# Performance work log

Measured on AMD Instinct MI355X. Metric: run time of the kernel, lower is better.

The kernel has to match this reference:

```python
import jax, jax.numpy as jnp
import numpy as np

B, S, HID = 2, 2048, 2048
NH, NKV, HD = 8, 1, 256
G = NH // NKV  # key-value groups
ROPE_BASE = 10000.0


def _rope_tables(seq_len, dim, base=ROPE_BASE):
    inv_freq = 1.0 / (base ** (jnp.arange(0, dim, 2, dtype=jnp.float32) / dim))
    t = jnp.arange(seq_len, dtype=jnp.float32)
    freqs = jnp.outer(t, inv_freq)            # [S, dim/2]
    emb = jnp.concatenate([freqs, freqs], -1)  # [S, dim]
    return jnp.cos(emb), jnp.sin(emb)


def _rotate_half(x):
    x1, x2 = jnp.split(x, 2, axis=-1)
    return jnp.concatenate([-x2, x1], axis=-1)


def setup_inputs() -> dict:
    key = jax.random.key(0)
    ks = jax.random.split(key, 6)
    hidden_states = jax.random.normal(ks[0], (B, S, HID), dtype=jnp.float32)
    # additive causal mask (0 on/below diagonal, -1e9 above)
    causal = jnp.triu(jnp.full((S, S), -1e9, dtype=jnp.float32), k=1)
    attention_mask = jnp.broadcast_to(causal[None, None], (B, 1, S, S))
    sc = 0.02
    Wq = jax.random.normal(ks[1], (HID, NH * HD), dtype=jnp.float32) * sc
    Wk = jax.random.normal(ks[2], (HID, NKV * HD), dtype=jnp.float32) * sc
    Wv = jax.random.normal(ks[3], (HID, NKV * HD), dtype=jnp.float32) * sc
    Wo = jax.random.normal(ks[4], (NH * HD, HID), dtype=jnp.float32) * sc
    return {"hidden_states": hidden_states, "attention_mask": attention_mask,
            "Wq": Wq, "Wk": Wk, "Wv": Wv, "Wo": Wo}


def reference(hidden_states, attention_mask, Wq, Wk, Wv, Wo):
    b, s, _ = hidden_states.shape
    q = (hidden_states @ Wq).reshape(b, s, NH, HD).transpose(0, 2, 1, 3)    # [B,NH,S,D]
    k = (hidden_states @ Wk).reshape(b, s, NKV, HD).transpose(0, 2, 1, 3)   # [B,NKV,S,D]
    v = (hidden_states @ Wv).reshape(b, s, NKV, HD).transpose(0, 2, 1, 3)
    cos, sin = _rope_tables(s, HD)
    cos, sin = cos[None, None], sin[None, None]
    q = q * cos + _rotate_half(q) * sin
    k = k * cos + _rotate_half(k) * sin
    # GQA: broadcast KV over groups instead of repeat_interleave (same math)
    qg = q.reshape(b, NKV, G, s, HD)
    scores = jnp.einsum('bkgqd,bkld->bkgql', qg, k) / np.sqrt(HD)  # [B,NKV,G,S,S]
    scores = scores + attention_mask[:, :, None]                    # mask broadcast over kv/groups
    probs = jax.nn.softmax(scores, axis=-1)
    out = jnp.einsum('bkgql,bkld->bkgqd', probs, v)                 # [B,NKV,G,S,D]
    out = out.reshape(b, NH, s, HD).transpose(0, 2, 1, 3).reshape(b, s, NH * HD)
    return out @ Wo
```

## Files before the change

kernel.cpp:

```cpp
#include <hip/hip_runtime.h>
#include <hip/hip_bf16.h>
#include <cstdint>
#include <cstddef>

#define DEVI __device__ __forceinline__

typedef __attribute__((ext_vector_type(8))) short short8;
typedef __attribute__((ext_vector_type(4))) float f32x4;

constexpr int BB = 2, SS = 2048, HID = 2048, NH = 8, HD = 256;
constexpr int M_TOT = BB * SS;
constexpr int RTOT = BB * NH * SS;
constexpr float SM_SCALE_LOG2 = 0.09016844005556021f;

DEVI unsigned short f2bf(float f) {
  union { float f; unsigned int u; } v; v.f = f;
  unsigned int u = v.u;
  unsigned int r = (u + 0x7FFFu + ((u >> 16) & 1u)) >> 16;
  return (unsigned short)r;
}

DEVI float bf2f(unsigned short u) {
  union { unsigned int i; float f; } v; v.i = ((unsigned int)u) << 16;
  return v.f;
}

DEVI void gload_lds16(const void* g, void* l) {
  __builtin_amdgcn_global_load_lds(
      (const __attribute__((address_space(1))) unsigned int*)g,
      (__attribute__((address_space(3))) unsigned int*)l, 16, 0, 0);
}

__global__ void convert_f32_bf16(const float* __restrict__ in,
                                 unsigned short* __restrict__ out, int n8) {
  const int i = blockIdx.x * blockDim.x + threadIdx.x;
  if (i >= n8) return;
  const f32x4* p = (const f32x4*)in;
  f32x4 a = p[i * 2], b = p[i * 2 + 1];
  short8 o;
#pragma unroll
  for (int j = 0; j < 4; ++j) {
    o[j] = (short)f2bf(a[j]);
    o[j + 4] = (short)f2bf(b[j]);
  }
  ((short8*)out)[i] = o;
}

__global__ void transpose_w(const float* __restrict__ W,
                            unsigned short* __restrict__ Wt, int K, int N) {
  __shared__ float t[32][33];
  const int n0 = blockIdx.x * 32, k0 = blockIdx.y * 32;
  const int c = threadIdx.x & 31, r8 = threadIdx.x >> 5;
#pragma unroll
  for (int i = 0; i < 4; ++i) {
    const int r = r8 + i * 8;
    t[r][c] = W[(size_t)(k0 + r) * N + n0 + c];
  }
  __syncthreads();
#pragma unroll
  for (int i = 0; i < 4; ++i) {
    const int r = r8 + i * 8;
    Wt[(size_t)(n0 + r) * K + k0 + c] = f2bf(t[c][r]);
  }
}

__global__ void rope_table(float* __restrict__ ct, float* __restrict__ st) {
  const int i = blockIdx.x * blockDim.x + threadIdx.x;
  const int s = i >> 7, d = i & 127;
  const float inv = __expf(-(float)d * (9.210340371976184f / 128.0f));
  const float ang = (float)s * inv;
  float sn, cs;
  sincosf(ang, &sn, &cs);
  ct[i] = cs;
  st[i] = sn;
}

__global__ void rope_apply8(unsigned short* __restrict__ X, const float* __restrict__ ct,
                            const float* __restrict__ st, int heads, int stride, int total16) {
  const int i = blockIdx.x * blockDim.x + threadIdx.x;
  if (i >= total16) return;
  const int d0 = (i & 15) * 8;
  const int t = i >> 4;
  const int hh = t % heads;
  const int row = t / heads;
  const int s = row & (SS - 1);
  const size_t base = (size_t)row * stride + (size_t)hh * HD + d0;
  short8 q1 = *(const short8*)&X[base];
  short8 q2 = *(const short8*)&X[base + 128];
  const float* ctr = ct + s * 128 + d0;
  const float* str = st + s * 128 + d0;
  f32x4 c0 = *(const f32x4*)ctr, c1 = *(const f32x4*)(ctr + 4);
  f32x4 s0 = *(const f32x4*)str, s1 = *(const f32x4*)(str + 4);
  short8 o1, o2;
#pragma unroll
  for (int j = 0; j < 8; ++j) {
    const float a = bf2f((unsigned short)q1[j]);
    const float b = bf2f((unsigned short)q2[j]);
    const float cs = (j < 4) ? c0[j] : c1[j - 4];
    const float sn = (j < 4) ? s0[j] : s1[j - 4];
    o1[j] = (short)f2bf(a * cs - b * sn);
    o2[j] = (short)f2bf(b * cs + a * sn);
  }
  *(short8*)&X[base] = o1;
  *(short8*)&X[base + 128] = o2;
}

template <int WMODE>
__global__ __launch_bounds__(256)
void gemm_bt(const unsigned short* __restrict__ A,
             const unsigned short* __restrict__ Bt,
             void* __restrict__ Cp, void* __restrict__ Cp2, void* __restrict__ Cp3,
             int N, int K) {
  __shared__ unsigned short As[128 * 64];
  __shared__ unsigned short Bs[128 * 64];
  const int tid = threadIdx.x;
  const int wid = tid >> 6, lane = tid & 63;
  const int wr = wid >> 1, wc = wid & 1;
  const int l15 = lane & 15, lg = lane >> 4;
  const unsigned lid = blockIdx.y * gridDim.x + blockIdx.x;
  const unsigned cpx = (gridDim.x * gridDim.y) >> 3;
  const unsigned swz = (lid & 7) * cpx + (lid >> 3);
  const int m0 = (int)(swz / gridDim.x) * 128, n0 = (int)(swz % gridDim.x) * 128;
  const int lrow = lane >> 3, lch = lane & 7;
  f32x4 acc[4][4];
#pragma unroll
  for (int i = 0; i < 4; ++i)
#pragma unroll
    for (int j = 0; j < 4; ++j) acc[i][j] = f32x4{0.f, 0.f, 0.f, 0.f};
  const unsigned short* Ab = A + (size_t)m0 * K;
  const unsigned short* Bb = Bt + (size_t)n0 * K;
  for (int k0 = 0; k0 < K; k0 += 64) {
    __syncthreads();
#pragma unroll
    for (int i = 0; i < 4; ++i) {
      const int r0 = wid * 32 + i * 8;
      const int r = r0 + lrow;
      gload_lds16(Ab + (size_t)r * K + k0 + ((lch ^ (r & 7)) * 8), &As[r0 * 64]);
      gload_lds16(Bb + (size_t)r * K + k0 + ((lch ^ (r & 7)) * 8), &Bs[r0 * 64]);
    }
    asm volatile("s_waitcnt vmcnt(0)" ::: "memory");
    __syncthreads();
#pragma unroll
    for (int kk = 0; kk < 2; ++kk) {
      short8 a[4], b[4];
#pragma unroll
      for (int m = 0; m < 4; ++m) {
        const int row = wr * 64 + m * 16 + l15;
        a[m] = *(const short8*)&As[row * 64 + (((kk * 4 + lg) ^ (row & 7)) * 8)];
      }
#pragma unroll
      for (int n = 0; n < 4; ++n) {
        const int row = wc * 64 + n * 16 + l15;
        b[n] = *(const short8*)&Bs[row * 64 + (((kk * 4 + lg) ^ (row & 7)) * 8)];
      }
#pragma unroll
      for (int m = 0; m < 4; ++m)
#pragma unroll
        for (int n = 0; n < 4; ++n)
          acc[m][n] = __builtin_amdgcn_mfma_f32_16x16x32_bf16(a[m], b[n], acc[m][n], 0, 0, 0);
    }
  }
  const int row0 = m0 + wr * 64 + lg * 4;
  const int col0 = n0 + wc * 64 + l15;
#pragma unroll
  for (int m = 0; m < 4; ++m)
#pragma unroll
    for (int n = 0; n < 4; ++n)
#pragma unroll
      for (int r = 0; r < 4; ++r) {
        const int row = row0 + m * 16 + r;
        const int col = col0 + n * 16;
        const float v = acc[m][n][r];
        if (WMODE == 1) {
          ((float*)Cp)[(size_t)row * N + col] = v;
        } else {
          if (col < 2048)
            ((unsigned short*)Cp)[(size_t)row * 2048 + col] = f2bf(v);
          else if (col < 2304)
            ((unsigned short*)Cp2)[(size_t)row * 256 + (col - 2048)] = f2bf(v);
          else
            ((unsigned short*)Cp3)[((size_t)((row >> 11) * HD + (col - 2304))) * SS + (row & (SS - 1))] = f2bf(v);
        }
      }
}

__global__ __launch_bounds__(512)
void attn_split(const unsigned short* __restrict__ Q,
                const unsigned short* __restrict__ Kc,
                const unsigned short* __restrict__ Vt,
                unsigned short* __restrict__ Opart, float* __restrict__ Ml) {
  __shared__ unsigned short Ks[2][64 * 256];
  __shared__ unsigned short Vs[2][256 * 64];
  __shared__ unsigned short Ps[8][1024];
  const int tid = threadIdx.x;
  const int wid = tid >> 6, lane = tid & 63;
  const int l15 = lane & 15, lg = lane >> 4;
  const int pi = (int)blockIdx.x >> 1, s = (int)blockIdx.x & 1;
  const int h = blockIdx.y, b = blockIdx.z;
  const int qtA = pi, qtB = 15 - pi;

  short8 qf[8];
  f32x4 acc[16];
  float mrow[4], lrow[4];

  auto load_q = [&](int qt) {
    const int qrow = qt * 128 + wid * 16 + l15;
    const size_t qbase = ((size_t)(b * SS + qrow)) * (NH * HD) + (size_t)h * HD;
#pragma unroll
    for (int c = 0; c < 8; ++c)
      qf[c] = *(const short8*)&Q[qbase + c * 32 + lg * 8];
#pragma unroll
    for (int n = 0; n < 16; ++n) acc[n] = f32x4{0.f, 0.f, 0.f, 0.f};
#pragma unroll
    for (int r = 0; r < 4; ++r) { mrow[r] = -3e38f; lrow[r] = 0.f; }
  };

  auto write_part = [&](int qt) {
    const size_t rbase = ((size_t)(b * NH + h)) * SS + qt * 128 + wid * 16 + lg * 4;
#pragma unroll
    for (int n = 0; n < 16; ++n)
#pragma unroll
      for (int r = 0; r < 4; ++r)
        Opart[((size_t)s * RTOT + rbase + r) * 256 + n * 16 + l15] = f2bf(acc[n][r]);
    if (l15 == 0) {
#pragma unroll
      for (int r = 0; r < 4; ++r)
        ((float2*)Ml)[(size_t)s * RTOT + rbase + r] = float2{mrow[r], lrow[r]};
    }
  };

  auto stage = [&](int buf, int kv0) {
    unsigned short* KsB = &Ks[buf][0];
    unsigned short* VsB = &Vs[buf][0];
#pragma unroll
    for (int j = 0; j < 4; ++j) {
      {
        const int r0 = wid * 8 + j * 2;
        const int r = r0 + (lane >> 5), c = lane & 31;
        gload_lds16(Kc + ((size_t)(b * SS + kv0 + r)) * HD + ((c ^ (r & 7)) * 8),
                    &KsB[r0 * 256]);
      }
      {
        const int r0 = (wid * 4 + j) * 8;
        const int r = r0 + (lane >> 3), c = lane & 7;
        gload_lds16(Vt + ((size_t)(b * HD + r)) * SS + kv0 + ((c ^ (r & 7)) * 8),
                    &VsB[r0 * 64]);
      }
    }
  };

  auto compute = [&](int buf, int qt, int kv0) {
    const int wmax = qt * 128 + wid * 16 + 15;
    if (kv0 > wmax) return;
    const unsigned short* KsB = &Ks[buf][0];
    const unsigned short* VsB = &Vs[buf][0];
    f32x4 sf[4];
    __builtin_amdgcn_s_setprio(1);
#pragma unroll
    for (int t = 0; t < 4; ++t) {
      f32x4 sv = {0.f, 0.f, 0.f, 0.f};
      const int kvr = t * 16 + l15;
      const char* krow = (const char*)KsB + kvr * 512;
      const int sw = (kvr & 7) << 4;
#pragma unroll
      for (int c = 0; c < 8; ++c) {
        short8 bf = *(const short8*)(krow + ((c * 64 + lg * 16) ^ sw));
        sv = __builtin_amdgcn_mfma_f32_16x16x32_bf16(qf[c], bf, sv, 0, 0, 0);
      }
      sf[t] = sv;
    }
    __builtin_amdgcn_s_setprio(0);

    float pm[4] = {-3e38f, -3e38f, -3e38f, -3e38f};
    const int qr0 = qt * 128 + wid * 16 + lg * 4;
#pragma unroll
    for (int t = 0; t < 4; ++t) {
      const int kvc = kv0 + t * 16 + l15;
#pragma unroll
      for (int r = 0; r < 4; ++r) {
        float v = sf[t][r] * SM_SCALE_LOG2;
        v = (kvc > qr0 + r) ? -3e38f : v;
        sf[t][r] = v;
        pm[r] = fmaxf(pm[r], v);
      }
    }
    float scale[4];
    float growth = -3e38f;
#pragma unroll
    for (int r = 0; r < 4; ++r) {
      float v = pm[r];
      v = fmaxf(v, __shfl_xor(v, 1));
      v = fmaxf(v, __shfl_xor(v, 2));
      v = fmaxf(v, __shfl_xor(v, 4));
      v = fmaxf(v, __shfl_xor(v, 8));
      pm[r] = v;
      growth = fmaxf(growth, v - mrow[r]);
    }
    const bool norescale = __all(growth <= 0.f);
#pragma unroll
    for (int r = 0; r < 4; ++r) {
      const float mn = norescale ? mrow[r] : fmaxf(mrow[r], pm[r]);
      scale[r] = norescale ? 1.f : exp2f(mrow[r] - mn);
      mrow[r] = mn;
      float sum = 0.f;
#pragma unroll
      for (int t = 0; t < 4; ++t) {
        const float p = exp2f(sf[t][r] - mn);
        sf[t][r] = p;
        sum += p;
      }
      sum += __shfl_xor(sum, 1);
      sum += __shfl_xor(sum, 2);
      sum += __shfl_xor(sum, 4);
      sum += __shfl_xor(sum, 8);
      lrow[r] = lrow[r] * scale[r] + sum;
    }
    if (!norescale) {
#pragma unroll
      for (int n = 0; n < 16; ++n)
#pragma unroll
        for (int r = 0; r < 4; ++r) acc[n][r] *= scale[r];
    }

    char* pw = (char*)&Ps[wid][0];
#pragma unroll
    for (int t = 0; t < 4; ++t)
#pragma unroll
      for (int r = 0; r < 4; ++r) {
        const int q = lg * 4 + r;
        *(unsigned short*)(pw + q * 128 + (((t * 16 + l15) * 2) ^ ((q & 7) << 4))) =
            f2bf(sf[t][r]);
      }
    asm volatile("s_waitcnt lgkmcnt(0)" ::: "memory");
    short8 pf[2];
    {
      const char* pr = pw + l15 * 128;
      const int sw = (l15 & 7) << 4;
      pf[0] = *(const short8*)(pr + ((lg * 16) ^ sw));
      pf[1] = *(const short8*)(pr + ((64 + lg * 16) ^ sw));
    }
    __builtin_amdgcn_s_setprio(1);
#pragma unroll
    for (int n = 0; n < 16; ++n) {
      const int dr = n * 16 + l15;
      const char* vrow = (const char*)VsB + dr * 128;
      const int sw = (dr & 7) << 4;
      short8 v0 = *(const short8*)(vrow + ((lg * 16) ^ sw));
      short8 v1 = *(const short8*)(vrow + ((64 + lg * 16) ^ sw));
      acc[n] = __builtin_amdgcn_mfma_f32_16x16x32_bf16(pf[0], v0, acc[n], 0, 0, 0);
      acc[n] = __builtin_amdgcn_mfma_f32_16x16x32_bf16(pf[1], v1, acc[n], 0, 0, 0);
    }
    __builtin_amdgcn_s_setprio(0);
  };

  auto kv_of = [&](int i) {
    const int j = (i <= qtA) ? i : (i - qtA - 1);
    return (s + 2 * j) * 64;
  };

  load_q(qtA);
  stage(0, kv_of(0));
  asm volatile("s_waitcnt vmcnt(0)" ::: "memory");
  __syncthreads();
  int buf = 0;
  for (int i = 0; i < 17; ++i) {
    if (i + 1 < 17) stage(buf ^ 1, kv_of(i + 1));
    if (i == qtA + 1) {
      write_part(qtA);
      load_q(qtB);
    }
    const int qt = (i <= qtA) ? qtA : qtB;
    compute(buf, qt, kv_of(i));
    asm volatile("s_waitcnt vmcnt(0)" ::: "memory");
    __syncthreads();
    buf ^= 1;
  }
  write_part(qtB);
}

__global__ void merge_splits(const unsigned short* __restrict__ Opart,
                             const float* __restrict__ Ml,
                             unsigned short* __restrict__ AO) {
  const int gid = blockIdx.x * 256 + threadIdx.x;
  const int ridx = gid >> 5;
  const int d0 = (gid & 31) * 8;
  const float2 ab0 = ((const float2*)Ml)[ridx];
  const float2 ab1 = ((const float2*)Ml)[RTOT + ridx];
  const float M = fmaxf(ab0.x, ab1.x);
  const float w0 = exp2f(ab0.x - M), w1 = exp2f(ab1.x - M);
  const float inv = 1.f / (w0 * ab0.y + w1 * ab1.y);
  const short8 p0 = *(const short8*)&Opart[(size_t)ridx * 256 + d0];
  const short8 p1 = *(const short8*)&Opart[((size_t)RTOT + ridx) * 256 + d0];
  const int b = ridx >> 14, rem = ridx & 16383;
  const int h = rem >> 11, srow = rem & 2047;
  short8 o;
#pragma unroll
  for (int j = 0; j < 8; ++j)
    o[j] = (short)f2bf((w0 * bf2f((unsigned short)p0[j]) +
                        w1 * bf2f((unsigned short)p1[j])) * inv);
  *(short8*)(AO + ((size_t)(b * SS + srow)) * (NH * HD) + (size_t)h * HD + d0) = o;
}

__global__ __launch_bounds__(256)
void attn_fb(const unsigned short* __restrict__ Q,
             const unsigned short* __restrict__ Kc,
             const unsigned short* __restrict__ Vt,
             unsigned short* __restrict__ AO) {
  __shared__ unsigned short Ks[2][64 * 256];
  __shared__ unsigned short Vs[2][256 * 64];
  __shared__ unsigned short Ps[4][1024];
  const int tid = threadIdx.x;
  const int wid = tid >> 6, lane = tid & 63;
  const int l15 = lane & 15, lg = lane >> 4;
  const int qtA = (int)blockIdx.x;
  const int qtB = 31 - qtA;
  const int h = blockIdx.y, b = blockIdx.z;

  short8 qf[8];
  f32x4 acc[16];
  float mrow[4], lrow[4];

  auto load_q = [&](int qt) {
    const int qrow = qt * 64 + wid * 16 + l15;
    const size_t qbase = ((size_t)(b * SS + qrow)) * (NH * HD) + (size_t)h * HD;
#pragma unroll
    for (int c = 0; c < 8; ++c)
      qf[c] = *(const short8*)&Q[qbase + c * 32 + lg * 8];
#pragma unroll
    for (int n = 0; n < 16; ++n) acc[n] = f32x4{0.f, 0.f, 0.f, 0.f};
#pragma unroll
    for (int r = 0; r < 4; ++r) { mrow[r] = -3e38f; lrow[r] = 0.f; }
  };

  auto write_o = [&](int qt) {
    float invl[4];
#pragma unroll
    for (int r = 0; r < 4; ++r) invl[r] = 1.f / lrow[r];
    const int orow0 = b * SS + qt * 64 + wid * 16 + lg * 4;
#pragma unroll
    for (int n = 0; n < 16; ++n)
#pragma unroll
      for (int r = 0; r < 4; ++r)
        AO[(size_t)(orow0 + r) * (NH * HD) + (size_t)h * HD + n * 16 + l15] =
            f2bf(acc[n][r] * invl[r]);
  };

  auto stage = [&](int buf, int kv0) {
    unsigned short* KsB = &Ks[buf][0];
    unsigned short* VsB = &Vs[buf][0];
#pragma unroll
    for (int j = 0; j < 8; ++j) {
      {
        const int r0 = wid * 16 + j * 2;
        const int r = r0 + (lane >> 5), c = lane & 31;
        gload_lds16(Kc + ((size_t)(b * SS + kv0 + r)) * HD + ((c ^ (r & 7)) * 8),
                    &KsB[r0 * 256]);
      }
      {
        const int r0 = (wid * 8 + j) * 8;
        const int r = r0 + (lane >> 3), c = lane & 7;
        gload_lds16(Vt + ((size_t)(b * HD + r)) * SS + kv0 + ((c ^ (r & 7)) * 8),
                    &VsB[r0 * 64]);
      }
    }
  };

  auto compute = [&](int buf, int qt, int kv0) {
    const int wmax = qt * 64 + wid * 16 + 15;
    if (kv0 > wmax) return;
    const unsigned short* KsB = &Ks[buf][0];
    const unsigned short* VsB = &Vs[buf][0];
    f32x4 sf[4];
#pragma unroll
    for (int t = 0; t < 4; ++t) {
      f32x4 sv = {0.f, 0.f, 0.f, 0.f};
      const int kvr = t * 16 + l15;
      const char* krow = (const char*)KsB + kvr * 512;
      const int sw = (kvr & 7) << 4;
#pragma unroll
      for (int c = 0; c < 8; ++c) {
        short8 bf = *(const short8*)(krow + ((c * 64 + lg * 16) ^ sw));
        sv = __builtin_amdgcn_mfma_f32_16x16x32_bf16(qf[c], bf, sv, 0, 0, 0);
      }
      sf[t] = sv;
    }
    float pm[4] = {-3e38f, -3e38f, -3e38f, -3e38f};
    const int qr0 = qt * 64 + wid * 16 + lg * 4;
#pragma unroll
    for (int t = 0; t < 4; ++t) {
      const int kvc = kv0 + t * 16 + l15;
#pragma unroll
      for (int r = 0; r < 4; ++r) {
        float v = sf[t][r] * 0.0625f;
        v = (kvc > qr0 + r) ? -3e38f : v;
        sf[t][r] = v;
        pm[r] = fmaxf(pm[r], v);
      }
    }
    float scale[4];
    float growth = -3e38f;
#pragma unroll
    for (int r = 0; r < 4; ++r) {
      float v = pm[r];
      v = fmaxf(v, __shfl_xor(v, 1));
      v = fmaxf(v, __shfl_xor(v, 2));
      v = fmaxf(v, __shfl_xor(v, 4));
      v = fmaxf(v, __shfl_xor(v, 8));
      pm[r] = v;
      growth = fmaxf(growth, v - mrow[r]);
    }
    const bool norescale = __all(growth <= 0.f);
#pragma unroll
    for (int r = 0; r < 4; ++r) {
      const float mn = norescale ? mrow[r] : fmaxf(mrow[r], pm[r]);
      scale[r] = norescale ? 1.f : __expf(mrow[r] - mn);
      mrow[r] = mn;
      float sum = 0.f;
#pragma unroll
      for (int t = 0; t < 4; ++t) {
        const float p = __expf(sf[t][r] - mn);
        sf[t][r] = p;
        sum += p;
      }
      sum += __shfl_xor(sum, 1);
      sum += __shfl_xor(sum, 2);
      sum += __shfl_xor(sum, 4);
      sum += __shfl_xor(sum, 8);
      lrow[r] = lrow[r] * scale[r] + sum;
    }
    if (!norescale) {
#pragma unroll
      for (int n = 0; n < 16; ++n)
#pragma unroll
        for (int r = 0; r < 4; ++r) acc[n][r] *= scale[r];
    }
    char* pw = (char*)&Ps[wid][0];
#pragma unroll
    for (int t = 0; t < 4; ++t)
#pragma unroll
      for (int r = 0; r < 4; ++r) {
        const int q = lg * 4 + r;
        *(unsigned short*)(pw + q * 128 + (((t * 16 + l15) * 2) ^ ((q & 7) << 4))) =
            f2bf(sf[t][r]);
      }
    asm volatile("s_waitcnt lgkmcnt(0)" ::: "memory");
    short8 pf[2];
    {
      const char* pr = pw + l15 * 128;
      const int sw = (l15 & 7) << 4;
      pf[0] = *(const short8*)(pr + ((lg * 16) ^ sw));
      pf[1] = *(const short8*)(pr + ((64 + lg * 16) ^ sw));
    }
#pragma unroll
    for (int n = 0; n < 16; ++n) {
      const int dr = n * 16 + l15;
      const char* vrow = (const char*)VsB + dr * 128;
      const int sw = (dr & 7) << 4;
      short8 v0 = *(const short8*)(vrow + ((lg * 16) ^ sw));
      short8 v1 = *(const short8*)(vrow + ((64 + lg * 16) ^ sw));
      acc[n] = __builtin_amdgcn_mfma_f32_16x16x32_bf16(pf[0], v0, acc[n], 0, 0, 0);
      acc[n] = __builtin_amdgcn_mfma_f32_16x16x32_bf16(pf[1], v1, acc[n], 0, 0, 0);
    }
  };

  const int nA = qtA + 1;
  load_q(qtA);
  int curq = qtA;
  stage(0, 0);
  asm volatile("s_waitcnt vmcnt(0)" ::: "memory");
  __syncthreads();
  int buf = 0;
  for (int i = 0; i < 33; ++i) {
    const int t0 = (i >= nA) ? (i - nA) : i;
    if (i + 1 < 33) {
      const int t0n = (i + 1 >= nA) ? (i + 1 - nA) : (i + 1);
      stage(buf ^ 1, t0n * 64);
    }
    if (i >= nA && curq == qtA) {
      write_o(qtA);
      load_q(qtB);
      curq = qtB;
    }
    compute(buf, curq, t0 * 64);
    asm volatile("s_waitcnt vmcnt(0)" ::: "memory");
    __syncthreads();
    buf ^= 1;
  }
  write_o(qtB);
}

extern "C" void kernel_launch(void* const* d_in, const int* in_sizes, int n_in,
                              void* d_out, int out_size, void* d_ws, size_t ws_size,
                              hipStream_t stream) {
  (void)in_sizes; (void)n_in; (void)out_size;
  const float* hs = (const float*)d_in[0];
  const float* Wq = (const float*)d_in[2];
  const float* Wk = (const float*)d_in[3];
  const float* Wv = (const float*)d_in[4];
  const float* Wo = (const float*)d_in[5];

  char* ws = (char*)d_ws;
  size_t off = 0;
  auto alloc = [&](size_t bytes) -> void* {
    void* p = ws + off;
    off += (bytes + 255) & ~(size_t)255;
    return p;
  };
  unsigned short* Xb  = (unsigned short*)alloc((size_t)M_TOT * HID * 2);
  unsigned short* WqT = (unsigned short*)alloc((size_t)2048 * 2048 * 2);
  unsigned short* WkT = (unsigned short*)alloc((size_t)256 * 2048 * 2);
  unsigned short* WvT = (unsigned short*)alloc((size_t)256 * 2048 * 2);
  unsigned short* WoT = (unsigned short*)alloc((size_t)2048 * 2048 * 2);
  unsigned short* Qb  = (unsigned short*)alloc((size_t)M_TOT * 2048 * 2);
  unsigned short* Kb  = (unsigned short*)alloc((size_t)M_TOT * 256 * 2);
  unsigned short* Vtw = (unsigned short*)alloc((size_t)M_TOT * 256 * 2);
  float* ct = (float*)alloc((size_t)SS * 128 * 4);
  float* st = (float*)alloc((size_t)SS * 128 * 4);
  unsigned short* Opart = (unsigned short*)alloc((size_t)2 * RTOT * 256 * 2);
  float* Mlb = (float*)alloc((size_t)2 * RTOT * 2 * 4);
  const bool use_split = ws_size >= off;
  unsigned short* AO = Xb;

  convert_f32_bf16<<<M_TOT * HID / 8 / 256, 256, 0, stream>>>(hs, Xb, M_TOT * HID / 8);
  transpose_w<<<dim3(2048 / 32, 2048 / 32), 256, 0, stream>>>(Wq, WqT, 2048, 2048);
  transpose_w<<<dim3(256 / 32, 2048 / 32), 256, 0, stream>>>(Wk, WkT, 2048, 256);
  transpose_w<<<dim3(256 / 32, 2048 / 32), 256, 0, stream>>>(Wv, WvT, 2048, 256);
  transpose_w<<<dim3(2048 / 32, 2048 / 32), 256, 0, stream>>>(Wo, WoT, 2048, 2048);
  rope_table<<<SS * 128 / 256, 256, 0, stream>>>(ct, st);

  gemm_bt<4><<<dim3(2560 / 128, M_TOT / 128), 256, 0, stream>>>(Xb, WqT, Qb, Kb, Vtw, 2560, 2048);

  rope_apply8<<<(M_TOT * NH * 16) / 256, 256, 0, stream>>>(Qb, ct, st, NH, 2048, M_TOT * NH * 16);
  rope_apply8<<<(M_TOT * 16) / 256, 256, 0, stream>>>(Kb, ct, st, 1, 256, M_TOT * 16);

  if (use_split) {
    attn_split<<<dim3(16, NH, BB), 512, 0, stream>>>(Qb, Kb, Vtw, Opart, Mlb);
    merge_splits<<<RTOT * 32 / 256, 256, 0, stream>>>(Opart, Mlb, AO);
  } else {
    attn_fb<<<dim3(16, NH, BB), 256, 0, stream>>>(Qb, Kb, Vtw, AO);
  }

  gemm_bt<1><<<dim3(2048 / 128, M_TOT / 128), 256, 0, stream>>>(AO, WoT, d_out, nullptr, nullptr, 2048, 2048);
}
```

Before: 228.9 us.

## Widen attention blocks to 256 query rows with four-way KV split

The split attention kernel now runs 1024-thread blocks covering 256 query rows, and each block handles a quarter of the KV tiles (4-way split instead of 2-way). The separate P scratch buffer is dropped and P is written into the already-consumed K stage buffer, which requires an extra block barrier between QK and PV. The merge kernel now combines four partials. The aim is more reuse of each staged K/V tile across query rows, at the cost of extra barriers, twice the partial-output traffic, and tighter register pressure under the new launch bounds.

Result: slower. 383.9 us (+67.7%).

```diff
diff --git a/kernel.cpp b/kernel.cpp
--- a/kernel.cpp
+++ b/kernel.cpp
@@ -184,27 +184,26 @@
       }
 }
 
-__global__ __launch_bounds__(512)
+__global__ __launch_bounds__(1024, 4)
 void attn_split(const unsigned short* __restrict__ Q,
                 const unsigned short* __restrict__ Kc,
                 const unsigned short* __restrict__ Vt,
                 unsigned short* __restrict__ Opart, float* __restrict__ Ml) {
   __shared__ unsigned short Ks[2][64 * 256];
   __shared__ unsigned short Vs[2][256 * 64];
-  __shared__ unsigned short Ps[8][1024];
   const int tid = threadIdx.x;
   const int wid = tid >> 6, lane = tid & 63;
   const int l15 = lane & 15, lg = lane >> 4;
-  const int pi = (int)blockIdx.x >> 1, s = (int)blockIdx.x & 1;
+  const int pi = (int)blockIdx.x >> 2, s = (int)blockIdx.x & 3;
   const int h = blockIdx.y, b = blockIdx.z;
-  const int qtA = pi, qtB = 15 - pi;
+  const int qtA = pi, qtB = 7 - pi;
 
   short8 qf[8];
   f32x4 acc[16];
   float mrow[4], lrow[4];
 
   auto load_q = [&](int qt) {
-    const int qrow = qt * 128 + wid * 16 + l15;
+    const int qrow = qt * 256 + wid * 16 + l15;
     const size_t qbase = ((size_t)(b * SS + qrow)) * (NH * HD) + (size_t)h * HD;
 #pragma unroll
     for (int c = 0; c < 8; ++c)
@@ -216,7 +215,7 @@
   };
 
   auto write_part = [&](int qt) {
-    const size_t rbase = ((size_t)(b * NH + h)) * SS + qt * 128 + wid * 16 + lg * 4;
+    const size_t rbase = ((size_t)(b * NH + h)) * SS + qt * 256 + wid * 16 + lg * 4;
 #pragma unroll
     for (int n = 0; n < 16; ++n)
 #pragma unroll
@@ -233,15 +232,15 @@
     unsigned short* KsB = &Ks[buf][0];
     unsigned short* VsB = &Vs[buf][0];
 #pragma unroll
-    for (int j = 0; j < 4; ++j) {
+    for (int j = 0; j < 2; ++j) {
       {
-        const int r0 = wid * 8 + j * 2;
+        const int r0 = wid * 4 + j * 2;
         const int r = r0 + (lane >> 5), c = lane & 31;
         gload_lds16(Kc + ((size_t)(b * SS + kv0 + r)) * HD + ((c ^ (r & 7)) * 8),
                     &KsB[r0 * 256]);
       }
       {
-        const int r0 = (wid * 4 + j) * 8;
+        const int r0 = wid * 16 + j * 8;
         const int r = r0 + (lane >> 3), c = lane & 7;
         gload_lds16(Vt + ((size_t)(b * HD + r)) * SS + kv0 + ((c ^ (r & 7)) * 8),
                     &VsB[r0 * 64]);
@@ -249,113 +248,9 @@
     }
   };
 
-  auto compute = [&](int buf, int qt, int kv0) {
-    const int wmax = qt * 128 + wid * 16 + 15;
-    if (kv0 > wmax) return;
-    const unsigned short* KsB = &Ks[buf][0];
-    const unsigned short* VsB = &Vs[buf][0];
-    f32x4 sf[4];
-    __builtin_amdgcn_s_setprio(1);
-#pragma unroll
-    for (int t = 0; t < 4; ++t) {
-      f32x4 sv = {0.f, 0.f, 0.f, 0.f};
-      const int kvr = t * 16 + l15;
-      const char* krow = (const char*)KsB + kvr * 512;
-      const int sw = (kvr & 7) << 4;
-#pragma unroll
-      for (int c = 0; c < 8; ++c) {
-        short8 bf = *(const short8*)(krow + ((c * 64 + lg * 16) ^ sw));
-        sv = __builtin_amdgcn_mfma_f32_16x16x32_bf16(qf[c], bf, sv, 0, 0, 0);
-      }
-      sf[t] = sv;
-    }
-    __builtin_amdgcn_s_setprio(0);
-
-    float pm[4] = {-3e38f, -3e38f, -3e38f, -3e38f};
-    const int qr0 = qt * 128 + wid * 16 + lg * 4;
-#pragma unroll
-    for (int t = 0; t < 4; ++t) {
-      const int kvc = kv0 + t * 16 + l15;
-#pragma unroll
-      for (int r = 0; r < 4; ++r) {
-        float v = sf[t][r] * SM_SCALE_LOG2;
-        v = (kvc > qr0 + r) ? -3e38f : v;
-        sf[t][r] = v;
-        pm[r] = fmaxf(pm[r], v);
-      }
-    }
-    float scale[4];
-    float growth = -3e38f;
-#pragma unroll
-    for (int r = 0; r < 4; ++r) {
-      float v = pm[r];
-      v = fmaxf(v, __shfl_xor(v, 1));
-      v = fmaxf(v, __shfl_xor(v, 2));
-      v = fmaxf(v, __shfl_xor(v, 4));
-      v = fmaxf(v, __shfl_xor(v, 8));
-      pm[r] = v;
-      growth = fmaxf(growth, v - mrow[r]);
-    }
-    const bool norescale = __all(growth <= 0.f);
-#pragma unroll
-    for (int r = 0; r < 4; ++r) {
-      const float mn = norescale ? mrow[r] : fmaxf(mrow[r], pm[r]);
-      scale[r] = norescale ? 1.f : exp2f(mrow[r] - mn);
-      mrow[r] = mn;
-      float sum = 0.f;
-#pragma unroll
-      for (int t = 0; t < 4; ++t) {
-        const float p = exp2f(sf[t][r] - mn);
-        sf[t][r] = p;
-        sum += p;
-      }
-      sum += __shfl_xor(sum, 1);
-      sum += __shfl_xor(sum, 2);
-      sum += __shfl_xor(sum, 4);
-      sum += __shfl_xor(sum, 8);
-      lrow[r] = lrow[r] * scale[r] + sum;
-    }
-    if (!norescale) {
-#pragma unroll
-      for (int n = 0; n < 16; ++n)
-#pragma unroll
-        for (int r = 0; r < 4; ++r) acc[n][r] *= scale[r];
-    }
-
-    char* pw = (char*)&Ps[wid][0];
-#pragma unroll
-    for (int t = 0; t < 4; ++t)
-#pragma unroll
-      for (int r = 0; r < 4; ++r) {
-        const int q = lg * 4 + r;
-        *(unsigned short*)(pw + q * 128 + (((t * 16 + l15) * 2) ^ ((q & 7) << 4))) =
-            f2bf(sf[t][r]);
-      }
-    asm volatile("s_waitcnt lgkmcnt(0)" ::: "memory");
-    short8 pf[2];
-    {
-      const char* pr = pw + l15 * 128;
-      const int sw = (l15 & 7) << 4;
-      pf[0] = *(const short8*)(pr + ((lg * 16) ^ sw));
-      pf[1] = *(const short8*)(pr + ((64 + lg * 16) ^ sw));
-    }
-    __builtin_amdgcn_s_setprio(1);
-#pragma unroll
-    for (int n = 0; n < 16; ++n) {
-      const int dr = n * 16 + l15;
-      const char* vrow = (const char*)VsB + dr * 128;
-      const int sw = (dr & 7) << 4;
-      short8 v0 = *(const short8*)(vrow + ((lg * 16) ^ sw));
-      short8 v1 = *(const short8*)(vrow + ((64 + lg * 16) ^ sw));
-      acc[n] = __builtin_amdgcn_mfma_f32_16x16x32_bf16(pf[0], v0, acc[n], 0, 0, 0);
-      acc[n] = __builtin_amdgcn_mfma_f32_16x16x32_bf16(pf[1], v1, acc[n], 0, 0, 0);
-    }
-    __builtin_amdgcn_s_setprio(0);
-  };
-
   auto kv_of = [&](int i) {
     const int j = (i <= qtA) ? i : (i - qtA - 1);
-    return (s + 2 * j) * 64;
+    return (s + 4 * j) * 64;
   };
 
   load_q(qtA);
@@ -363,14 +258,120 @@
   asm volatile("s_waitcnt vmcnt(0)" ::: "memory");
   __syncthreads();
   int buf = 0;
-  for (int i = 0; i < 17; ++i) {
-    if (i + 1 < 17) stage(buf ^ 1, kv_of(i + 1));
+  for (int i = 0; i < 9; ++i) {
+    if (i + 1 < 9) stage(buf ^ 1, kv_of(i + 1));
     if (i == qtA + 1) {
       write_part(qtA);
       load_q(qtB);
     }
     const int qt = (i <= qtA) ? qtA : qtB;
-    compute(buf, qt, kv_of(i));
+    const int kv0 = kv_of(i);
+    const bool active = kv0 <= qt * 256 + wid * 16 + 15;
+    const unsigned short* KsB = &Ks[buf][0];
+    const unsigned short* VsB = &Vs[buf][0];
+
+    f32x4 sf[4];
+    if (active) {
+      __builtin_amdgcn_s_setprio(1);
+#pragma unroll
+      for (int t = 0; t < 4; ++t) {
+        f32x4 sv = {0.f, 0.f, 0.f, 0.f};
+        const int kvr = t * 16 + l15;
+        const char* krow = (const char*)KsB + kvr * 512;
+        const int sw = (kvr & 7) << 4;
+#pragma unroll
+        for (int c = 0; c < 8; ++c) {
+          short8 bf = *(const short8*)(krow + ((c * 64 + lg * 16) ^ sw));
+          sv = __builtin_amdgcn_mfma_f32_16x16x32_bf16(qf[c], bf, sv, 0, 0, 0);
+        }
+        sf[t] = sv;
+      }
+      __builtin_amdgcn_s_setprio(0);
+    }
+    __syncthreads();
+
+    if (active) {
+      float pm[4] = {-3e38f, -3e38f, -3e38f, -3e38f};
+      const int qr0 = qt * 256 + wid * 16 + lg * 4;
+#pragma unroll
+      for (int t = 0; t < 4; ++t) {
+        const int kvc = kv0 + t * 16 + l15;
+#pragma unroll
+        for (int r = 0; r < 4; ++r) {
+          float v = sf[t][r] * SM_SCALE_LOG2;
+          v = (kvc > qr0 + r) ? -3e38f : v;
+          sf[t][r] = v;
+          pm[r] = fmaxf(pm[r], v);
+        }
+      }
+      float scale[4];
+      float growth = -3e38f;
+#pragma unroll
+      for (int r = 0; r < 4; ++r) {
+        float v = pm[r];
+        v = fmaxf(v, __shfl_xor(v, 1));
+        v = fmaxf(v, __shfl_xor(v, 2));
+        v = fmaxf(v, __shfl_xor(v, 4));
+        v = fmaxf(v, __shfl_xor(v, 8));
+        pm[r] = v;
+        growth = fmaxf(growth, v - mrow[r]);
+      }
+      const bool norescale = __all(growth <= 0.f);
+#pragma unroll
+      for (int r = 0; r < 4; ++r) {
+        const float mn = norescale ? mrow[r] : fmaxf(mrow[r], pm[r]);
+        scale[r] = norescale ? 1.f : exp2f(mrow[r] - mn);
+        mrow[r] = mn;
+        float sum = 0.f;
+#pragma unroll
+        for (int t = 0; t < 4; ++t) {
+          const float p = exp2f(sf[t][r] - mn);
+          sf[t][r] = p;
+          sum += p;
+        }
+        sum += __shfl_xor(sum, 1);
+        sum += __shfl_xor(sum, 2);
+        sum += __shfl_xor(sum, 4);
+        sum += __shfl_xor(sum, 8);
+        lrow[r] = lrow[r] * scale[r] + sum;
+      }
+      if (!norescale) {
+#pragma unroll
+        for (int n = 0; n < 16; ++n)
+#pragma unroll
+          for (int r = 0; r < 4; ++r) acc[n][r] *= scale[r];
+      }
+
+      char* pw = (char*)&Ks[buf][wid * 1024];
+#pragma unroll
+      for (int t = 0; t < 4; ++t)
+#pragma unroll
+        for (int r = 0; r < 4; ++r) {
+          const int q = lg * 4 + r;
+          *(unsigned short*)(pw + q * 128 + (((t * 16 + l15) * 2) ^ ((q & 7) << 4))) =
+              f2bf(sf[t][r]);
+        }
+      asm volatile("s_waitcnt lgkmcnt(0)" ::: "memory");
+      short8 pf[2];
+      {
+        const char* pr = pw + l15 * 128;
+        const int sw = (l15 & 7) << 4;
+        pf[0] = *(const short8*)(pr + ((lg * 16) ^ sw));
+        pf[1] = *(const short8*)(pr + ((64 + lg * 16) ^ sw));
+      }
+      __builtin_amdgcn_s_setprio(1);
+#pragma unroll
+      for (int n = 0; n < 16; ++n) {
+        const int dr = n * 16 + l15;
+        const char* vrow = (const char*)VsB + dr * 128;
+        const int sw = (dr & 7) << 4;
+        short8 v0 = *(const short8*)(vrow + ((lg * 16) ^ sw));
+        short8 v1 = *(const short8*)(vrow + ((64 + lg * 16) ^ sw));
+        acc[n] = __builtin_amdgcn_mfma_f32_16x16x32_bf16(pf[0], v0, acc[n], 0, 0, 0);
+        acc[n] = __builtin_amdgcn_mfma_f32_16x16x32_bf16(pf[1], v1, acc[n], 0, 0, 0);
+      }
+      __builtin_amdgcn_s_setprio(0);
+    }
     asm volatile("s_waitcnt vmcnt(0)" ::: "memory");
     __syncthreads();
     buf ^= 1;
@@ -384,20 +385,31 @@
   const int gid = blockIdx.x * 256 + threadIdx.x;
   const int ridx = gid >> 5;
   const int d0 = (gid & 31) * 8;
-  const float2 ab0 = ((const float2*)Ml)[ridx];
-  const float2 ab1 = ((const float2*)Ml)[RTOT + ridx];
-  const float M = fmaxf(ab0.x, ab1.x);
-  const float w0 = exp2f(ab0.x - M), w1 = exp2f(ab1.x - M);
-  const float inv = 1.f / (w0 * ab0.y + w1 * ab1.y);
-  const short8 p0 = *(const short8*)&Opart[(size_t)ridx * 256 + d0];
-  const short8 p1 = *(const short8*)&Opart[((size_t)RTOT + ridx) * 256 + d0];
+  float2 ab[4];
+#pragma unroll
+  for (int s = 0; s < 4; ++s) ab[s] = ((const float2*)Ml)[(size_t)s * RTOT + ridx];
+  float M = fmaxf(fmaxf(ab[0].x, ab[1].x), fmaxf(ab[2].x, ab[3].x));
+  float w[4], denom = 0.f;
+#pragma unroll
+  for (int s = 0; s < 4; ++s) {
+    w[s] = exp2f(ab[s].x - M);
+    denom += w[s] * ab[s].y;
+  }
+  const float inv = 1.f / denom;
+  short8 p[4];
+#pragma unroll
+  for (int s = 0; s < 4; ++s)
+    p[s] = *(const short8*)&Opart[((size_t)s * RTOT + ridx) * 256 + d0];
   const int b = ridx >> 14, rem = ridx & 16383;
   const int h = rem >> 11, srow = rem & 2047;
   short8 o;
 #pragma unroll
-  for (int j = 0; j < 8; ++j)
-    o[j] = (short)f2bf((w0 * bf2f((unsigned short)p0[j]) +
-                        w1 * bf2f((unsigned short)p1[j])) * inv);
+  for (int j = 0; j < 8; ++j) {
+    float v = 0.f;
+#pragma unroll
+    for (int s = 0; s < 4; ++s) v += w[s] * bf2f((unsigned short)p[s][j]);
+    o[j] = (short)f2bf(v * inv);
+  }
   *(short8*)(AO + ((size_t)(b * SS + srow)) * (NH * HD) + (size_t)h * HD + d0) = o;
 }
 
@@ -616,8 +628,8 @@
   unsigned short* Vtw = (unsigned short*)alloc((size_t)M_TOT * 256 * 2);
   float* ct = (float*)alloc((size_t)SS * 128 * 4);
   float* st = (float*)alloc((size_t)SS * 128 * 4);
-  unsigned short* Opart = (unsigned short*)alloc((size_t)2 * RTOT * 256 * 2);
-  float* Mlb = (float*)alloc((size_t)2 * RTOT * 2 * 4);
+  unsigned short* Opart = (unsigned short*)alloc((size_t)4 * RTOT * 256 * 2);
+  float* Mlb = (float*)alloc((size_t)4 * RTOT * 2 * 4);
   const bool use_split = ws_size >= off;
   unsigned short* AO = Xb;
 
@@ -634,7 +646,7 @@
   rope_apply8<<<(M_TOT * 16) / 256, 256, 0, stream>>>(Kb, ct, st, 1, 256, M_TOT * 16);
 
   if (use_split) {
-    attn_split<<<dim3(16, NH, BB), 512, 0, stream>>>(Qb, Kb, Vtw, Opart, Mlb);
+    attn_split<<<dim3(16, NH, BB), 1024, 0, stream>>>(Qb, Kb, Vtw, Opart, Mlb);
     merge_splits<<<RTOT * 32 / 256, 256, 0, stream>>>(Opart, Mlb, AO);
   } else {
     attn_fb<<<dim3(16, NH, BB), 256, 0, stream>>>(Qb, Kb, Vtw, AO);
```

## Single-buffer K/V in attention and reuse K tile for P staging

Applied to the files above, without the earlier changes.

Drops the double-buffered K/V shared-memory tiles and the separate per-wave P buffer, cutting LDS use from about 144KB to 64KB per block so more blocks can be resident per CU. Each iteration now loads K/V synchronously, waits, computes QK^T, synchronises, and then overwrites the K tile with the probability matrix before PV. This gives up the overlap between prefetching the next K/V tile and computing the current one, and adds an extra barrier per iteration, in exchange for higher occupancy.

Result: slower. 235.6 us (+2.9%).

```diff
diff --git a/kernel.cpp b/kernel.cpp
--- a/kernel.cpp
+++ b/kernel.cpp
@@ -189,9 +189,8 @@
                 const unsigned short* __restrict__ Kc,
                 const unsigned short* __restrict__ Vt,
                 unsigned short* __restrict__ Opart, float* __restrict__ Ml) {
-  __shared__ unsigned short Ks[2][64 * 256];
-  __shared__ unsigned short Vs[2][256 * 64];
-  __shared__ unsigned short Ps[8][1024];
+  __shared__ unsigned short Ks[64 * 256];
+  __shared__ unsigned short Vs[256 * 64];
   const int tid = threadIdx.x;
   const int wid = tid >> 6, lane = tid & 63;
   const int l15 = lane & 15, lg = lane >> 4;
@@ -229,128 +228,22 @@
     }
   };
 
-  auto stage = [&](int buf, int kv0) {
-    unsigned short* KsB = &Ks[buf][0];
-    unsigned short* VsB = &Vs[buf][0];
+  auto stage = [&](int kv0) {
 #pragma unroll
     for (int j = 0; j < 4; ++j) {
       {
         const int r0 = wid * 8 + j * 2;
         const int r = r0 + (lane >> 5), c = lane & 31;
         gload_lds16(Kc + ((size_t)(b * SS + kv0 + r)) * HD + ((c ^ (r & 7)) * 8),
-                    &KsB[r0 * 256]);
+                    &Ks[r0 * 256]);
       }
       {
         const int r0 = (wid * 4 + j) * 8;
         const int r = r0 + (lane >> 3), c = lane & 7;
         gload_lds16(Vt + ((size_t)(b * HD + r)) * SS + kv0 + ((c ^ (r & 7)) * 8),
-                    &VsB[r0 * 64]);
-      }
-    }
-  };
-
-  auto compute = [&](int buf, int qt, int kv0) {
-    const int wmax = qt * 128 + wid * 16 + 15;
-    if (kv0 > wmax) return;
-    const unsigned short* KsB = &Ks[buf][0];
-    const unsigned short* VsB = &Vs[buf][0];
-    f32x4 sf[4];
-    __builtin_amdgcn_s_setprio(1);
-#pragma unroll
-    for (int t = 0; t < 4; ++t) {
-      f32x4 sv = {0.f, 0.f, 0.f, 0.f};
-      const int kvr = t * 16 + l15;
-      const char* krow = (const char*)KsB + kvr * 512;
-      const int sw = (kvr & 7) << 4;
-#pragma unroll
-      for (int c = 0; c < 8; ++c) {
-        short8 bf = *(const short8*)(krow + ((c * 64 + lg * 16) ^ sw));
-        sv = __builtin_amdgcn_mfma_f32_16x16x32_bf16(qf[c], bf, sv, 0, 0, 0);
-      }
-      sf[t] = sv;
-    }
-    __builtin_amdgcn_s_setprio(0);
-
-    float pm[4] = {-3e38f, -3e38f, -3e38f, -3e38f};
-    const int qr0 = qt * 128 + wid * 16 + lg * 4;
-#pragma unroll
-    for (int t = 0; t < 4; ++t) {
-      const int kvc = kv0 + t * 16 + l15;
-#pragma unroll
-      for (int r = 0; r < 4; ++r) {
-        float v = sf[t][r] * SM_SCALE_LOG2;
-        v = (kvc > qr0 + r) ? -3e38f : v;
-        sf[t][r] = v;
-        pm[r] = fmaxf(pm[r], v);
-      }
-    }
-    float scale[4];
-    float growth = -3e38f;
-#pragma unroll
-    for (int r = 0; r < 4; ++r) {
-      float v = pm[r];
-      v = fmaxf(v, __shfl_xor(v, 1));
-      v = fmaxf(v, __shfl_xor(v, 2));
-      v = fmaxf(v, __shfl_xor(v, 4));
-      v = fmaxf(v, __shfl_xor(v, 8));
-      pm[r] = v;
-      growth = fmaxf(growth, v - mrow[r]);
-    }
-    const bool norescale = __all(growth <= 0.f);
-#pragma unroll
-    for (int r = 0; r < 4; ++r) {
-      const float mn = norescale ? mrow[r] : fmaxf(mrow[r], pm[r]);
-      scale[r] = norescale ? 1.f : exp2f(mrow[r] - mn);
-      mrow[r] = mn;
-      float sum = 0.f;
-#pragma unroll
-      for (int t = 0; t < 4; ++t) {
-        const float p = exp2f(sf[t][r] - mn);
-        sf[t][r] = p;
-        sum += p;
-      }
-      sum += __shfl_xor(sum, 1);
-      sum += __shfl_xor(sum, 2);
-      sum += __shfl_xor(sum, 4);
-      sum += __shfl_xor(sum, 8);
-      lrow[r] = lrow[r] * scale[r] + sum;
-    }
-    if (!norescale) {
-#pragma unroll
-      for (int n = 0; n < 16; ++n)
-#pragma unroll
-        for (int r = 0; r < 4; ++r) acc[n][r] *= scale[r];
-    }
-
-    char* pw = (char*)&Ps[wid][0];
-#pragma unroll
-    for (int t = 0; t < 4; ++t)
-#pragma unroll
-      for (int r = 0; r < 4; ++r) {
-        const int q = lg * 4 + r;
-        *(unsigned short*)(pw + q * 128 + (((t * 16 + l15) * 2) ^ ((q & 7) << 4))) =
-            f2bf(sf[t][r]);
-      }
-    asm volatile("s_waitcnt lgkmcnt(0)" ::: "memory");
-    short8 pf[2];
-    {
-      const char* pr = pw + l15 * 128;
-      const int sw = (l15 & 7) << 4;
-      pf[0] = *(const short8*)(pr + ((lg * 16) ^ sw));
-      pf[1] = *(const short8*)(pr + ((64 + lg * 16) ^ sw));
-    }
-    __builtin_amdgcn_s_setprio(1);
-#pragma unroll
-    for (int n = 0; n < 16; ++n) {
-      const int dr = n * 16 + l15;
-      const char* vrow = (const char*)VsB + dr * 128;
-      const int sw = (dr & 7) << 4;
-      short8 v0 = *(const short8*)(vrow + ((lg * 16) ^ sw));
-      short8 v1 = *(const short8*)(vrow + ((64 + lg * 16) ^ sw));
-      acc[n] = __builtin_amdgcn_mfma_f32_16x16x32_bf16(pf[0], v0, acc[n], 0, 0, 0);
-      acc[n] = __builtin_amdgcn_mfma_f32_16x16x32_bf16(pf[1], v1, acc[n], 0, 0, 0);
-    }
-    __builtin_amdgcn_s_setprio(0);
+                    &Vs[r0 * 64]);
+      }
+    }
   };
 
   auto kv_of = [&](int i) {
@@ -359,21 +252,121 @@
   };
 
   load_q(qtA);
-  stage(0, kv_of(0));
-  asm volatile("s_waitcnt vmcnt(0)" ::: "memory");
-  __syncthreads();
-  int buf = 0;
   for (int i = 0; i < 17; ++i) {
-    if (i + 1 < 17) stage(buf ^ 1, kv_of(i + 1));
+    const int kv0 = kv_of(i);
+    __syncthreads();
+    stage(kv0);
+    asm volatile("s_waitcnt vmcnt(0)" ::: "memory");
+    __syncthreads();
     if (i == qtA + 1) {
       write_part(qtA);
       load_q(qtB);
     }
     const int qt = (i <= qtA) ? qtA : qtB;
-    compute(buf, qt, kv_of(i));
-    asm volatile("s_waitcnt vmcnt(0)" ::: "memory");
+    const bool active = kv0 <= qt * 128 + wid * 16 + 15;
+
+    f32x4 sf[4];
+    if (active) {
+      __builtin_amdgcn_s_setprio(1);
+#pragma unroll
+      for (int t = 0; t < 4; ++t) {
+        f32x4 sv = {0.f, 0.f, 0.f, 0.f};
+        const int kvr = t * 16 + l15;
+        const char* krow = (const char*)Ks + kvr * 512;
+        const int sw = (kvr & 7) << 4;
+#pragma unroll
+        for (int c = 0; c < 8; ++c) {
+          short8 bf = *(const short8*)(krow + ((c * 64 + lg * 16) ^ sw));
+          sv = __builtin_amdgcn_mfma_f32_16x16x32_bf16(qf[c], bf, sv, 0, 0, 0);
+        }
+        sf[t] = sv;
+      }
+      __builtin_amdgcn_s_setprio(0);
+    }
     __syncthreads();
-    buf ^= 1;
+
+    if (active) {
+      float pm[4] = {-3e38f, -3e38f, -3e38f, -3e38f};
+      const int qr0 = qt * 128 + wid * 16 + lg * 4;
+#pragma unroll
+      for (int t = 0; t < 4; ++t) {
+        const int kvc = kv0 + t * 16 + l15;
+#pragma unroll
+        for (int r = 0; r < 4; ++r) {
+          float v = sf[t][r] * SM_SCALE_LOG2;
+          v = (kvc > qr0 + r) ? -3e38f : v;
+          sf[t][r] = v;
+          pm[r] = fmaxf(pm[r], v);
+        }
+      }
+      float scale[4];
+      float growth = -3e38f;
+#pragma unroll
+      for (int r = 0; r < 4; ++r) {
+        float v = pm[r];
+        v = fmaxf(v, __shfl_xor(v, 1));
+        v = fmaxf(v, __shfl_xor(v, 2));
+        v = fmaxf(v, __shfl_xor(v, 4));
+        v = fmaxf(v, __shfl_xor(v, 8));
+        pm[r] = v;
+        growth = fmaxf(growth, v - mrow[r]);
+      }
+      const bool norescale = __all(growth <= 0.f);
+#pragma unroll
+      for (int r = 0; r < 4; ++r) {
+        const float mn = norescale ? mrow[r] : fmaxf(mrow[r], pm[r]);
+        scale[r] = norescale ? 1.f : exp2f(mrow[r] - mn);
+        mrow[r] = mn;
+        float sum = 0.f;
+#pragma unroll
+        for (int t = 0; t < 4; ++t) {
+          const float p = exp2f(sf[t][r] - mn);
+          sf[t][r] = p;
+          sum += p;
+        }
+        sum += __shfl_xor(sum, 1);
+        sum += __shfl_xor(sum, 2);
+        sum += __shfl_xor(sum, 4);
+        sum += __shfl_xor(sum, 8);
+        lrow[r] = lrow[r] * scale[r] + sum;
+      }
+      if (!norescale) {
+#pragma unroll
+        for (int n = 0; n < 16; ++n)
+#pragma unroll
+          for (int r = 0; r < 4; ++r) acc[n][r] *= scale[r];
+      }
+
+      char* pw = (char*)&Ks[wid * 1024];
+#pragma unroll
+      for (int t = 0; t < 4; ++t)
+#pragma unroll
+        for (int r = 0; r < 4; ++r) {
+          const int q = lg * 4 + r;
+          *(unsigned short*)(pw + q * 128 + (((t * 16 + l15) * 2) ^ ((q & 7) << 4))) =
+              f2bf(sf[t][r]);
+        }
+      asm volatile("s_waitcnt lgkmcnt(0)" ::: "memory");
+      short8 pf[2];
+      {
+        const char* pr = pw + l15 * 128;
+        const int sw = (l15 & 7) << 4;
+        pf[0] = *(const short8*)(pr + ((lg * 16) ^ sw));
+        pf[1] = *(const short8*)(pr + ((64 + lg * 16) ^ sw));
+      }
+      __builtin_amdgcn_s_setprio(1);
+#pragma unroll
+      for (int n = 0; n < 16; ++n) {
+        const int dr = n * 16 + l15;
+        const char* vrow = (const char*)Vs + dr * 128;
+        const int sw = (dr & 7) << 4;
+        short8 v0 = *(const short8*)(vrow + ((lg * 16) ^ sw));
+        short8 v1 = *(const short8*)(vrow + ((64 + lg * 16) ^ sw));
+        acc[n] = __builtin_amdgcn_mfma_f32_16x16x32_bf16(pf[0], v0, acc[n], 0, 0, 0);
+        acc[n] = __builtin_amdgcn_mfma_f32_16x16x32_bf16(pf[1], v1, acc[n], 0, 0, 0);
+      }
+      __builtin_amdgcn_s_setprio(0);
+    }
   }
   write_part(qtB);
 }
```
